# Kernel optimization log

Measured on AMD Instinct MI355X. Metric: run time of the kernel, lower is better.

The kernel has to match this reference:

```python
import jax, jax.numpy as jnp
import numpy as np

D_IN = 1024
D_OUT = 1024
NUM_HEADS = 16
D_HEAD = D_OUT // NUM_HEADS


def setup_inputs() -> dict:
    key = jax.random.key(0)
    ks = jax.random.split(key, 6)
    s = 0.02
    return {
        "x": jax.random.normal(ks[0], (2, 2048, D_IN), dtype=jnp.float32),
        "W_q": jax.random.normal(ks[1], (D_IN, D_OUT), dtype=jnp.float32) * s,
        "W_k": jax.random.normal(ks[2], (D_IN, D_OUT), dtype=jnp.float32) * s,
        "W_v": jax.random.normal(ks[3], (D_IN, D_OUT), dtype=jnp.float32) * s,
        "W_o": jax.random.normal(ks[4], (D_OUT, D_OUT), dtype=jnp.float32) * s,
        "b_o": jax.random.normal(ks[5], (D_OUT,), dtype=jnp.float32) * s,
    }


def reference(x, W_q, W_k, W_v, W_o, b_o):
    B, T, _ = x.shape
    # qkv projections (no bias), split heads -> [B, H, T, d_head]
    def split_heads(t):
        return t.reshape(B, T, NUM_HEADS, D_HEAD).transpose(0, 2, 1, 3)
    q = split_heads(x @ W_q)
    k = split_heads(x @ W_k)
    v = split_heads(x @ W_v)
    # full causal scores [B, H, T, T]
    scores = jnp.einsum("bhqd,bhkd->bhqk", q, k)
    causal = jnp.triu(jnp.ones((T, T), dtype=bool), k=1)
    scores = jnp.where(causal, -jnp.inf, scores)
    attn = jax.nn.softmax(scores / np.sqrt(D_HEAD).astype(np.float32), axis=-1)
    # dropout rate is 0.0 -> identity
    ctx = jnp.einsum("bhqk,bhkd->bhqd", attn, v)
    ctx = ctx.transpose(0, 2, 1, 3).reshape(B, T, D_OUT)
    return ctx @ W_o + b_o
```

## Files before the change

### kernel.cpp

```cpp
#include <hip/hip_runtime.h>
#include <hip/hip_bf16.h>
#include <cstdint>

#define SEQ_T 2048
#define DMODEL 1024
#define NHEAD 16
#define DHEAD 64

typedef __attribute__((ext_vector_type(8))) __bf16 bf16x8;
typedef __attribute__((ext_vector_type(4))) float floatx4;
typedef __attribute__((ext_vector_type(16))) float floatx16;
typedef __attribute__((ext_vector_type(2))) unsigned uint32x2;

static __device__ __forceinline__ uint16_t f2bf(float f) {
    union { float f; uint32_t u; } v; v.f = f;
    uint32_t r = v.u + 0x7FFFu + ((v.u >> 16) & 1u);
    return (uint16_t)(r >> 16);
}

static __device__ __forceinline__ uint32_t pack2bf(float a, float b) {
    union { __bf16 h[2]; uint32_t u; } p;
    p.h[0] = (__bf16)a; p.h[1] = (__bf16)b;
    return p.u;
}

__global__ void mha_cvt(const float* __restrict__ x, uint16_t* __restrict__ xb,
                        const float* __restrict__ W0, const float* __restrict__ W1,
                        const float* __restrict__ W2, const float* __restrict__ W3,
                        uint16_t* __restrict__ T0, uint16_t* __restrict__ T1,
                        uint16_t* __restrict__ T2, uint16_t* __restrict__ T3) {
    if (blockIdx.z == 4) {
        int base = (blockIdx.y * 16 + blockIdx.x) * 256 + threadIdx.x;
#pragma unroll
        for (int i = 0; i < 16; ++i) {
            int idx = base + i * 65536;
            float4 f = ((const float4*)x)[idx];
            union { uint16_t u[4]; uint64_t v; } o;
            o.u[0] = f2bf(f.x); o.u[1] = f2bf(f.y); o.u[2] = f2bf(f.z); o.u[3] = f2bf(f.w);
            ((uint64_t*)xb)[idx] = o.v;
        }
        return;
    }
    const float* W; uint16_t* Tt; float sc;
    switch (blockIdx.z) {
        case 0: W = W0; Tt = T0; sc = 0.125f * 1.44269504089f; break;
        case 1: W = W1; Tt = T1; sc = 1.f; break;
        case 2: W = W2; Tt = T2; sc = 1.f; break;
        default: W = W3; Tt = T3; sc = 1.f; break;
    }
    __shared__ float tile[64][65];
    const int c  = threadIdx.x & 63;
    const int r0 = threadIdx.x >> 6;
    const int R0 = blockIdx.y * 64, C0 = blockIdx.x * 64;
#pragma unroll
    for (int rr = 0; rr < 16; ++rr) {
        int r = r0 + rr * 4;
        tile[r][c] = W[(size_t)(R0 + r) * DMODEL + C0 + c];
    }
    __syncthreads();
#pragma unroll
    for (int rr = 0; rr < 16; ++rr) {
        int r = r0 + rr * 4;
        Tt[(size_t)(C0 + r) * DMODEL + R0 + c] = f2bf(tile[c][r] * sc);
    }
}

template<int MODE>
__device__ __forceinline__ void gemm_bk64_body(
    const uint16_t* __restrict__ A, const uint16_t* __restrict__ Bt,
    uint16_t* __restrict__ outB) {
    const int K = DMODEL, N = DMODEL;
    extern __shared__ char smem[];
    uint16_t* As = (uint16_t*)smem;
    uint16_t* Bs = (uint16_t*)(smem + 8192);
    const int tid  = threadIdx.x;
    const int wave = tid >> 6;
    const int lane = tid & 63;
    const int m0 = blockIdx.y * 64;
    const int n0 = blockIdx.x * 128;
    const int lr   = lane & 15;
    const int quad = lane >> 4;

    floatx4 acc[4][2];
#pragma unroll
    for (int i = 0; i < 4; ++i)
#pragma unroll
        for (int j = 0; j < 2; ++j) acc[i][j] = (floatx4)0.0f;

    for (int k0 = 0; k0 < K; k0 += 64) {
#pragma unroll
        for (int i = 0; i < 2; ++i) {
            int c = i * 256 + tid;
            int r = c >> 3, s = (c & 7) ^ (r & 7);
            const uint16_t* g = A + (size_t)(m0 + r) * K + k0 + s * 8;
            __builtin_amdgcn_global_load_lds((const __attribute__((address_space(1))) void*)g,
                                             (__attribute__((address_space(3))) void*)(As + (size_t)c * 8), 16, 0, 0);
        }
#pragma unroll
        for (int i = 0; i < 4; ++i) {
            int c = i * 256 + tid;
            int r = c >> 3, s = (c & 7) ^ (r & 7);
            const uint16_t* g = Bt + (size_t)(n0 + r) * K + k0 + s * 8;
            __builtin_amdgcn_global_load_lds((const __attribute__((address_space(1))) void*)g,
                                             (__attribute__((address_space(3))) void*)(Bs + (size_t)c * 8), 16, 0, 0);
        }
        __syncthreads();
#pragma unroll
        for (int ks = 0; ks < 2; ++ks) {
            bf16x8 af[4], bfr[2];
#pragma unroll
            for (int mi = 0; mi < 4; ++mi) {
                int row = mi * 16 + lr;
                af[mi] = *(const bf16x8*)&As[row * 64 + (((ks * 4 + quad) ^ (row & 7)) << 3)];
            }
#pragma unroll
            for (int ni = 0; ni < 2; ++ni) {
                int row = wave * 32 + ni * 16 + lr;
                bfr[ni] = *(const bf16x8*)&Bs[row * 64 + (((ks * 4 + quad) ^ (row & 7)) << 3)];
            }
#pragma unroll
            for (int mi = 0; mi < 4; ++mi)
#pragma unroll
                for (int ni = 0; ni < 2; ++ni)
                    acc[mi][ni] = __builtin_amdgcn_mfma_f32_16x16x32_bf16(af[mi], bfr[ni], acc[mi][ni], 0, 0, 0);
        }
        __syncthreads();
    }
    if constexpr (MODE == 1) {
        uint16_t* Ct = (uint16_t*)smem;
        const int bb = m0 >> 11, t0 = m0 & 2047;
#pragma unroll
        for (int mi = 0; mi < 4; ++mi)
#pragma unroll
            for (int ni = 0; ni < 2; ++ni) {
                int cl = wave * 32 + ni * 16 + lr;
                int tl = mi * 16 + quad * 4;
                int tls = tl ^ ((cl & 3) << 4);
                union { uint16_t u[4]; uint64_t v8; } pk;
#pragma unroll
                for (int r = 0; r < 4; ++r) pk.u[r] = f2bf(acc[mi][ni][r]);
                *(uint64_t*)&Ct[cl * 72 + tls] = pk.v8;
            }
        __syncthreads();
#pragma unroll
        for (int k = 0; k < 4; ++k) {
            int c = k * 256 + tid;
            int cl = c >> 3, off = (c & 7) * 8;
            int offs = off ^ ((cl & 3) << 4);
            uint4 v = *(const uint4*)&Ct[cl * 72 + offs];
            *(uint4*)&outB[((size_t)(bb * 1024 + n0 + cl)) * 2048 + t0 + off] = v;
        }
    } else {
#pragma unroll
        for (int mi = 0; mi < 4; ++mi)
#pragma unroll
            for (int ni = 0; ni < 2; ++ni) {
                int col = n0 + wave * 32 + ni * 16 + lr;
#pragma unroll
                for (int r = 0; r < 4; ++r) {
                    int row = m0 + mi * 16 + quad * 4 + r;
                    outB[(size_t)row * N + col] = f2bf(acc[mi][ni][r]);
                }
            }
    }
}

__global__ __launch_bounds__(256) void mha_gemm_qkv(
    const uint16_t* __restrict__ A,
    const uint16_t* __restrict__ Wq, const uint16_t* __restrict__ Wk, const uint16_t* __restrict__ Wv,
    uint16_t* __restrict__ Q, uint16_t* __restrict__ K, uint16_t* __restrict__ Vt) {
    switch (blockIdx.z) {
        case 0:  gemm_bk64_body<0>(A, Wq, Q);  break;
        case 1:  gemm_bk64_body<0>(A, Wk, K);  break;
        default: gemm_bk64_body<1>(A, Wv, Vt); break;
    }
}

__global__ __launch_bounds__(512) void mha_gemm_out(
    const uint16_t* __restrict__ A, const uint16_t* __restrict__ Wot,
    float* __restrict__ out, const float* __restrict__ bias) {
    const int K = DMODEL, N = DMODEL;
    extern __shared__ char smem[];
    uint16_t* As = (uint16_t*)smem;
    uint16_t* Bs = (uint16_t*)(smem + 8192);
    const int tid  = threadIdx.x;
    const int wave = tid >> 6;
    const int lane = tid & 63;
    const int m0 = blockIdx.y * 64;
    const int n0 = blockIdx.x * 128;
    const int lr   = lane & 15;
    const int quad = lane >> 4;
    const int wm = wave >> 2, wn = wave & 3;

    floatx4 acc[2][2];
#pragma unroll
    for (int i = 0; i < 2; ++i)
#pragma unroll
        for (int j = 0; j < 2; ++j) acc[i][j] = (floatx4)0.0f;

    for (int k0 = 0; k0 < K; k0 += 64) {
        {
            int c = tid;
            int r = c >> 3, s = (c & 7) ^ (r & 7);
            const uint16_t* g = A + (size_t)(m0 + r) * K + k0 + s * 8;
            __builtin_amdgcn_global_load_lds((const __attribute__((address_space(1))) void*)g,
                                             (__attribute__((address_space(3))) void*)(As + (size_t)c * 8), 16, 0, 0);
        }
#pragma unroll
        for (int i = 0; i < 2; ++i) {
            int c = i * 512 + tid;
            int r = c >> 3, s = (c & 7) ^ (r & 7);
            const uint16_t* g = Wot + (size_t)(n0 + r) * K + k0 + s * 8;
            __builtin_amdgcn_global_load_lds((const __attribute__((address_space(1))) void*)g,
                                             (__attribute__((address_space(3))) void*)(Bs + (size_t)c * 8), 16, 0, 0);
        }
        __syncthreads();
#pragma unroll
        for (int ks = 0; ks < 2; ++ks) {
            bf16x8 af[2], bfr[2];
#pragma unroll
            for (int mi = 0; mi < 2; ++mi) {
                int row = wm * 32 + mi * 16 + lr;
                af[mi] = *(const bf16x8*)&As[row * 64 + (((ks * 4 + quad) ^ (row & 7)) << 3)];
            }
#pragma unroll
            for (int ni = 0; ni < 2; ++ni) {
                int row = wn * 32 + ni * 16 + lr;
                bfr[ni] = *(const bf16x8*)&Bs[row * 64 + (((ks * 4 + quad) ^ (row & 7)) << 3)];
            }
#pragma unroll
            for (int mi = 0; mi < 2; ++mi)
#pragma unroll
                for (int ni = 0; ni < 2; ++ni)
                    acc[mi][ni] = __builtin_amdgcn_mfma_f32_16x16x32_bf16(af[mi], bfr[ni], acc[mi][ni], 0, 0, 0);
        }
        __syncthreads();
    }
#pragma unroll
    for (int mi = 0; mi < 2; ++mi)
#pragma unroll
        for (int ni = 0; ni < 2; ++ni) {
            int col = n0 + wn * 32 + ni * 16 + lr;
            float bv = bias[col];
#pragma unroll
            for (int r = 0; r < 4; ++r) {
                int row = m0 + wm * 32 + mi * 16 + quad * 4 + r;
                out[(size_t)row * N + col] = acc[mi][ni][r] + bv;
            }
        }
}

__global__ __launch_bounds__(256, 4) void mha_attn_mfma(
    const uint16_t* __restrict__ Q, const uint16_t* __restrict__ K,
    const uint16_t* __restrict__ Vt, uint16_t* __restrict__ ctx) {
    __shared__ alignas(16) uint16_t Ks[2][128 * 64];
    __shared__ alignas(16) uint16_t Vs[2][64 * 128];

    const int tid  = threadIdx.x;
    const int wave = tid >> 6;
    const int lane = tid & 63;
    const int l31  = lane & 31;
    const int hi   = lane >> 5;
    const int l7   = lane & 7;
    const int qg   = wave & 1;
    const int kvh  = wave >> 1;
    const int h = blockIdx.x;
    const int p = blockIdx.y;
    const int b = blockIdx.z;
    const int jH = 31 - p, jL = p;
    const int TH = (jH + 2) >> 1;

    const uint16_t* kg[4];
    const uint16_t* vg[4];
    int cch[4];
#pragma unroll
    for (int i = 0; i < 4; ++i) {
        int c = i * 256 + tid; cch[i] = c;
        int rk = c >> 3, ck = c & 7;
        kg[i] = K + ((size_t)(b * SEQ_T) + rk) * DMODEL + h * DHEAD + (ck ^ (rk & 7)) * 8;
        int rv = c >> 4, cv = c & 15;
        int sv = (cv & 8) | ((cv & 7) ^ (rv & 7));
        vg[i] = Vt + ((size_t)(b * 1024 + h * DHEAD + rv)) * 2048 + sv * 8;
    }

    int q0w = jH * 64 + qg * 32;
    bf16x8 qf[4];
    auto load_q = [&]() {
        const uint16_t* qb = Q + ((size_t)(b * SEQ_T) + q0w + l31) * DMODEL + h * DHEAD;
#pragma unroll
        for (int f = 0; f < 4; ++f)
            qf[f] = *(const bf16x8*)(qb + f * 16 + hi * 8);
    };
    load_q();

    floatx16 o[2];
#pragma unroll
    for (int dt = 0; dt < 2; ++dt) o[dt] = (floatx16)0.0f;
    float lac = 0.f;

    auto stage = [&](int kv0, int buf) {
#pragma unroll
        for (int i = 0; i < 4; ++i) {
            __builtin_amdgcn_global_load_lds(
                (const __attribute__((address_space(1))) void*)(kg[i] + (size_t)kv0 * DMODEL),
                (__attribute__((address_space(3))) void*)(&Ks[buf][cch[i] * 8]), 16, 0, 0);
            __builtin_amdgcn_global_load_lds(
                (const __attribute__((address_space(1))) void*)(vg[i] + kv0),
                (__attribute__((address_space(3))) void*)(&Vs[buf][cch[i] * 8]), 16, 0, 0);
        }
    };

    auto halfsum = [&](float x) -> float {
#if __has_builtin(__builtin_amdgcn_permlane32_swap)
        uint32x2 r = __builtin_amdgcn_permlane32_swap(__float_as_uint(x), __float_as_uint(x), false, false);
        return __uint_as_float(r.x) + __uint_as_float(r.y);
#else
        return x + __shfl_xor(x, 32, 64);
#endif
    };

    auto combine_store = [&](int cur) {
        __syncthreads();
        float* osc = (float*)&Vs[cur][0];
        float* lsc = (float*)&Ks[cur][0];
        float lt = halfsum(lac);
        if (kvh == 1) {
            if (lane < 32) lsc[qg * 32 + lane] = lt;
#pragma unroll
            for (int dt = 0; dt < 2; ++dt)
#pragma unroll
                for (int r = 0; r < 16; ++r) {
                    int row = (r & 3) + 8 * (r >> 2) + 4 * hi;
                    osc[(qg * 32 + row) * 64 + dt * 32 + l31] = o[dt][r];
                }
        }
        __syncthreads();
        if (kvh == 0) {
            float ltot = lt + lsc[qg * 32 + l31];
            if (lane < 32) lsc[64 + qg * 32 + lane] = 1.f / ltot;
#pragma unroll
            for (int dt = 0; dt < 2; ++dt)
#pragma unroll
                for (int r = 0; r < 16; ++r) {
                    int row = (r & 3) + 8 * (r >> 2) + 4 * hi;
                    float ov = o[dt][r] + osc[(qg * 32 + row) * 64 + dt * 32 + l31];
                    float li = lsc[64 + qg * 32 + row];
                    size_t addr = ((size_t)(b * SEQ_T) + q0w + row) * DMODEL + h * DHEAD + dt * 32 + l31;
                    ctx[addr] = f2bf(ov * li);
                }
        }
    };

    stage(0, 0);
    __syncthreads();

    for (int t = 0; t < 17; ++t) {
        const int cur = t & 1;
        const int kv0 = (t < TH ? t : t - TH) * 128;
        if (t + 1 < 17) {
            int tn = t + 1;
            stage((tn < TH ? tn : tn - TH) * 128, tn & 1);
        }
#pragma unroll
        for (int kt = 0; kt < 2; ++kt) {
            const int kb = kv0 + kvh * 64 + kt * 32;
            floatx16 s = (floatx16)0.0f;
#pragma unroll
            for (int f = 0; f < 4; ++f) {
                bf16x8 kf = *(const bf16x8*)&Ks[cur][(kvh * 64 + kt * 32 + l31) * 64 + (((2 * f + hi) ^ l7) << 3)];
                s = __builtin_amdgcn_mfma_f32_32x32x16_bf16(kf, qf[f], s, 0, 0, 0);
            }
            if (kb + 31 > q0w) {
                int qr = q0w + l31;
#pragma unroll
                for (int r = 0; r < 16; ++r) {
                    int k = kb + (r & 3) + 8 * (r >> 2) + 4 * hi;
                    if (k > qr) s[r] = -3e38f;
                }
            }
            float se[16];
#pragma unroll
            for (int r = 0; r < 16; ++r) {
                se[r] = __builtin_amdgcn_exp2f(s[r]);
                lac += se[r];
            }
            uint32_t d0[2], d1[2], d2[2], d3[2];
#pragma unroll
            for (int i = 0; i < 2; ++i) {
                d0[i] = pack2bf(se[2 * i],      se[2 * i + 1]);
                d1[i] = pack2bf(se[4 + 2 * i],  se[4 + 2 * i + 1]);
                d2[i] = pack2bf(se[8 + 2 * i],  se[8 + 2 * i + 1]);
                d3[i] = pack2bf(se[12 + 2 * i], se[12 + 2 * i + 1]);
            }
            bf16x8 paf[2];
#if __has_builtin(__builtin_amdgcn_permlane32_swap)
            {
                uint32x2 r0 = __builtin_amdgcn_permlane32_swap(d0[0], d1[0], false, false);
                uint32x2 r1 = __builtin_amdgcn_permlane32_swap(d0[1], d1[1], false, false);
                union { uint32_t u[4]; bf16x8 v; } f0;
                f0.u[0] = r0.x; f0.u[1] = r1.x; f0.u[2] = r0.y; f0.u[3] = r1.y;
                paf[0] = f0.v;
                uint32x2 r2 = __builtin_amdgcn_permlane32_swap(d2[0], d3[0], false, false);
                uint32x2 r3 = __builtin_amdgcn_permlane32_swap(d2[1], d3[1], false, false);
                union { uint32_t u[4]; bf16x8 v; } f1;
                f1.u[0] = r2.x; f1.u[1] = r3.x; f1.u[2] = r2.y; f1.u[3] = r3.y;
                paf[1] = f1.v;
            }
#else
            {
                uint32_t s00 = __shfl_xor((int)d0[0], 32, 64), s01 = __shfl_xor((int)d0[1], 32, 64);
                uint32_t s10 = __shfl_xor((int)d1[0], 32, 64), s11 = __shfl_xor((int)d1[1], 32, 64);
                union { uint32_t u[4]; bf16x8 v; } f0;
                f0.u[0] = hi ? s10 : d0[0]; f0.u[1] = hi ? s11 : d0[1];
                f0.u[2] = hi ? d1[0] : s00; f0.u[3] = hi ? d1[1] : s01;
                paf[0] = f0.v;
                uint32_t s20 = __shfl_xor((int)d2[0], 32, 64), s21 = __shfl_xor((int)d2[1], 32, 64);
                uint32_t s30 = __shfl_xor((int)d3[0], 32, 64), s31 = __shfl_xor((int)d3[1], 32, 64);
                union { uint32_t u[4]; bf16x8 v; } f1;
                f1.u[0] = hi ? s30 : d2[0]; f1.u[1] = hi ? s31 : d2[1];
                f1.u[2] = hi ? d3[0] : s20; f1.u[3] = hi ? d3[1] : s21;
                paf[1] = f1.v;
            }
#endif
#pragma unroll
            for (int f = 0; f < 2; ++f)
#pragma unroll
                for (int dt = 0; dt < 2; ++dt) {
                    bf16x8 vf = *(const bf16x8*)&Vs[cur][(dt * 32 + l31) * 128 + ((kvh * 8 + ((kt * 4 + 2 * f + hi) ^ l7)) << 3)];
                    o[dt] = __builtin_amdgcn_mfma_f32_32x32x16_bf16(paf[f], vf, o[dt], 0, 0, 0);
                }
        }
        if (t == TH - 1) {
            combine_store(cur);
            q0w = jL * 64 + qg * 32;
            load_q();
#pragma unroll
            for (int dt = 0; dt < 2; ++dt) o[dt] = (floatx16)0.0f;
            lac = 0.f;
        }
        if (t + 1 < 17) __syncthreads();
    }
    combine_store(0);
}

extern "C" void kernel_launch(void* const* d_in, const int* in_sizes, int n_in,
                              void* d_out, int out_size, void* d_ws, size_t ws_size,
                              hipStream_t stream) {
    const float* x  = (const float*)d_in[0];
    const float* Wq = (const float*)d_in[1];
    const float* Wk = (const float*)d_in[2];
    const float* Wv = (const float*)d_in[3];
    const float* Wo = (const float*)d_in[4];
    const float* bo = (const float*)d_in[5];
    float* out = (float*)d_out;

    char* ws = (char*)d_ws;
    const size_t SZ_X = (size_t)4096 * DMODEL * 2;
    const size_t SZ_W = (size_t)DMODEL * DMODEL * 2;
    size_t off = 0;
    uint16_t* xb  = (uint16_t*)(ws + off); off += SZ_X;
    uint16_t* wqt = (uint16_t*)(ws + off); off += SZ_W;
    uint16_t* wkt = (uint16_t*)(ws + off); off += SZ_W;
    uint16_t* wvt = (uint16_t*)(ws + off); off += SZ_W;
    uint16_t* wot = (uint16_t*)(ws + off); off += SZ_W;
    uint16_t* Qb  = (uint16_t*)(ws + off); off += SZ_X;
    uint16_t* Kb  = (uint16_t*)(ws + off); off += SZ_X;
    uint16_t* Vtb = (uint16_t*)(ws + off); off += SZ_X;
    uint16_t* Cb  = (uint16_t*)(ws + off); off += SZ_X;
    (void)ws_size; (void)in_sizes; (void)n_in; (void)out_size;

    mha_cvt<<<dim3(16, 16, 5), 256, 0, stream>>>(x, xb, Wq, Wk, Wv, Wo, wqt, wkt, wvt, wot);
    mha_gemm_qkv<<<dim3(8, 64, 3), 256, 24576, stream>>>(xb, wqt, wkt, wvt, Qb, Kb, Vtb);
    mha_attn_mfma<<<dim3(NHEAD, 16, 2), 256, 0, stream>>>(Qb, Kb, Vtb, Cb);
    mha_gemm_out<<<dim3(8, 64), 512, 24576, stream>>>(Cb, wot, out, bo);
}
```

Before: 175.1 us.

## Split attention KV tile across four wave pairs with 512-thread blocks

The attention kernel now runs 8 waves per block instead of 4. Each 128-key tile is split into four 32-key slices, one per wave pair, and each wave now handles a single 32-key sub-tile per iteration instead of two. Partial outputs and row sums are reduced through LDS in three serialized passes. It also wraps the MFMA sections in s_setprio to favour matrix issue. The aim is more waves in flight to hide latency, at the cost of a longer cross-wave reduction, more barriers and possibly lower occupancy from 64KB of dynamic LDS per block.

```diff
diff --git a/kernel.cpp b/kernel.cpp
--- a/kernel.cpp
+++ b/kernel.cpp
@@ -250,11 +250,12 @@
         }
 }
 
-__global__ __launch_bounds__(256, 4) void mha_attn_mfma(
+__global__ __launch_bounds__(512, 4) void mha_attn_mfma(
     const uint16_t* __restrict__ Q, const uint16_t* __restrict__ K,
     const uint16_t* __restrict__ Vt, uint16_t* __restrict__ ctx) {
-    __shared__ alignas(16) uint16_t Ks[2][128 * 64];
-    __shared__ alignas(16) uint16_t Vs[2][64 * 128];
+    extern __shared__ char asmem[];
+    uint16_t* Ks0 = (uint16_t*)asmem;
+    uint16_t* Vs0 = (uint16_t*)(asmem + 32768);
 
     const int tid  = threadIdx.x;
     const int wave = tid >> 6;
@@ -263,21 +264,21 @@
     const int hi   = lane >> 5;
     const int l7   = lane & 7;
     const int qg   = wave & 1;
-    const int kvh  = wave >> 1;
+    const int kvq  = wave >> 1;
     const int h = blockIdx.x;
     const int p = blockIdx.y;
     const int b = blockIdx.z;
     const int jH = 31 - p, jL = p;
-    const int TH = (jH + 2) >> 1;
-
-    const uint16_t* kg[4];
-    const uint16_t* vg[4];
-    int cch[4];
-#pragma unroll
-    for (int i = 0; i < 4; ++i) {
-        int c = i * 256 + tid; cch[i] = c;
+    const int TH = (33 - p) >> 1;
+
+    const uint16_t* kg[2];
+    const uint16_t* vg[2];
+    int cch[2];
+#pragma unroll
+    for (int i = 0; i < 2; ++i) {
+        int c = i * 512 + tid; cch[i] = c;
         int rk = c >> 3, ck = c & 7;
-        kg[i] = K + ((size_t)(b * SEQ_T) + rk) * DMODEL + h * DHEAD + (ck ^ (rk & 7)) * 8;
+        kg[i] = K + ((size_t)(b * SEQ_T) + rk) * DMODEL + h * DHEAD + ((ck ^ (rk & 7)) * 8);
         int rv = c >> 4, cv = c & 15;
         int sv = (cv & 8) | ((cv & 7) ^ (rv & 7));
         vg[i] = Vt + ((size_t)(b * 1024 + h * DHEAD + rv)) * 2048 + sv * 8;
@@ -299,14 +300,16 @@
     float lac = 0.f;
 
     auto stage = [&](int kv0, int buf) {
-#pragma unroll
-        for (int i = 0; i < 4; ++i) {
+        uint16_t* kd = Ks0 + buf * 8192;
+        uint16_t* vd = Vs0 + buf * 8192;
+#pragma unroll
+        for (int i = 0; i < 2; ++i) {
             __builtin_amdgcn_global_load_lds(
                 (const __attribute__((address_space(1))) void*)(kg[i] + (size_t)kv0 * DMODEL),
-                (__attribute__((address_space(3))) void*)(&Ks[buf][cch[i] * 8]), 16, 0, 0);
+                (__attribute__((address_space(3))) void*)(kd + cch[i] * 8), 16, 0, 0);
             __builtin_amdgcn_global_load_lds(
                 (const __attribute__((address_space(1))) void*)(vg[i] + kv0),
-                (__attribute__((address_space(3))) void*)(&Vs[buf][cch[i] * 8]), 16, 0, 0);
+                (__attribute__((address_space(3))) void*)(vd + cch[i] * 8), 16, 0, 0);
         }
     };
 
@@ -321,21 +324,35 @@
 
     auto combine_store = [&](int cur) {
         __syncthreads();
-        float* osc = (float*)&Vs[cur][0];
-        float* lsc = (float*)&Ks[cur][0];
+        float* osc = (float*)(Ks0 + cur * 8192);
+        float* lsc = (float*)(Vs0 + cur * 8192);
         float lt = halfsum(lac);
-        if (kvh == 1) {
-            if (lane < 32) lsc[qg * 32 + lane] = lt;
-#pragma unroll
-            for (int dt = 0; dt < 2; ++dt)
-#pragma unroll
-                for (int r = 0; r < 16; ++r) {
-                    int row = (r & 3) + 8 * (r >> 2) + 4 * hi;
-                    osc[(qg * 32 + row) * 64 + dt * 32 + l31] = o[dt][r];
+#pragma unroll
+        for (int pass = 3; pass >= 1; --pass) {
+            if (kvq == pass) {
+                if (pass == 3) {
+#pragma unroll
+                    for (int dt = 0; dt < 2; ++dt)
+#pragma unroll
+                        for (int r = 0; r < 16; ++r) {
+                            int row = (r & 3) + 8 * (r >> 2) + 4 * hi;
+                            osc[(qg * 32 + row) * 64 + dt * 32 + l31] = o[dt][r];
+                        }
+                    if (lane < 32) lsc[qg * 32 + lane] = lt;
+                } else {
+#pragma unroll
+                    for (int dt = 0; dt < 2; ++dt)
+#pragma unroll
+                        for (int r = 0; r < 16; ++r) {
+                            int row = (r & 3) + 8 * (r >> 2) + 4 * hi;
+                            osc[(qg * 32 + row) * 64 + dt * 32 + l31] += o[dt][r];
+                        }
+                    if (lane < 32) lsc[qg * 32 + lane] += lt;
                 }
-        }
-        __syncthreads();
-        if (kvh == 0) {
+            }
+            __syncthreads();
+        }
+        if (kvq == 0) {
             float ltot = lt + lsc[qg * 32 + l31];
             if (lane < 32) lsc[64 + qg * 32 + lane] = 1.f / ltot;
 #pragma unroll
@@ -361,75 +378,78 @@
             int tn = t + 1;
             stage((tn < TH ? tn : tn - TH) * 128, tn & 1);
         }
-#pragma unroll
-        for (int kt = 0; kt < 2; ++kt) {
-            const int kb = kv0 + kvh * 64 + kt * 32;
-            floatx16 s = (floatx16)0.0f;
-#pragma unroll
-            for (int f = 0; f < 4; ++f) {
-                bf16x8 kf = *(const bf16x8*)&Ks[cur][(kvh * 64 + kt * 32 + l31) * 64 + (((2 * f + hi) ^ l7) << 3)];
-                s = __builtin_amdgcn_mfma_f32_32x32x16_bf16(kf, qf[f], s, 0, 0, 0);
-            }
-            if (kb + 31 > q0w) {
-                int qr = q0w + l31;
-#pragma unroll
-                for (int r = 0; r < 16; ++r) {
-                    int k = kb + (r & 3) + 8 * (r >> 2) + 4 * hi;
-                    if (k > qr) s[r] = -3e38f;
-                }
-            }
-            float se[16];
+        const uint16_t* Kc = Ks0 + cur * 8192;
+        const uint16_t* Vc = Vs0 + cur * 8192;
+        const int kb = kv0 + kvq * 32;
+        floatx16 s = (floatx16)0.0f;
+        __builtin_amdgcn_s_setprio(1);
+#pragma unroll
+        for (int f = 0; f < 4; ++f) {
+            bf16x8 kf = *(const bf16x8*)&Kc[(kvq * 32 + l31) * 64 + (((2 * f + hi) ^ l7) << 3)];
+            s = __builtin_amdgcn_mfma_f32_32x32x16_bf16(kf, qf[f], s, 0, 0, 0);
+        }
+        __builtin_amdgcn_s_setprio(0);
+        if (kb + 31 > q0w) {
+            int qr = q0w + l31;
 #pragma unroll
             for (int r = 0; r < 16; ++r) {
-                se[r] = __builtin_amdgcn_exp2f(s[r]);
-                lac += se[r];
-            }
-            uint32_t d0[2], d1[2], d2[2], d3[2];
-#pragma unroll
-            for (int i = 0; i < 2; ++i) {
-                d0[i] = pack2bf(se[2 * i],      se[2 * i + 1]);
-                d1[i] = pack2bf(se[4 + 2 * i],  se[4 + 2 * i + 1]);
-                d2[i] = pack2bf(se[8 + 2 * i],  se[8 + 2 * i + 1]);
-                d3[i] = pack2bf(se[12 + 2 * i], se[12 + 2 * i + 1]);
-            }
-            bf16x8 paf[2];
+                int k = kb + (r & 3) + 8 * (r >> 2) + 4 * hi;
+                if (k > qr) s[r] = -3e38f;
+            }
+        }
+        float se[16];
+#pragma unroll
+        for (int r = 0; r < 16; ++r) {
+            se[r] = __builtin_amdgcn_exp2f(s[r]);
+            lac += se[r];
+        }
+        uint32_t d0[2], d1[2], d2[2], d3[2];
+#pragma unroll
+        for (int i = 0; i < 2; ++i) {
+            d0[i] = pack2bf(se[2 * i],      se[2 * i + 1]);
+            d1[i] = pack2bf(se[4 + 2 * i],  se[4 + 2 * i + 1]);
+            d2[i] = pack2bf(se[8 + 2 * i],  se[8 + 2 * i + 1]);
+            d3[i] = pack2bf(se[12 + 2 * i], se[12 + 2 * i + 1]);
+        }
+        bf16x8 paf[2];
 #if __has_builtin(__builtin_amdgcn_permlane32_swap)
-            {
-                uint32x2 r0 = __builtin_amdgcn_permlane32_swap(d0[0], d1[0], false, false);
-                uint32x2 r1 = __builtin_amdgcn_permlane32_swap(d0[1], d1[1], false, false);
-                union { uint32_t u[4]; bf16x8 v; } f0;
-                f0.u[0] = r0.x; f0.u[1] = r1.x; f0.u[2] = r0.y; f0.u[3] = r1.y;
-                paf[0] = f0.v;
-                uint32x2 r2 = __builtin_amdgcn_permlane32_swap(d2[0], d3[0], false, false);
-                uint32x2 r3 = __builtin_amdgcn_permlane32_swap(d2[1], d3[1], false, false);
-                union { uint32_t u[4]; bf16x8 v; } f1;
-                f1.u[0] = r2.x; f1.u[1] = r3.x; f1.u[2] = r2.y; f1.u[3] = r3.y;
-                paf[1] = f1.v;
-            }
+        {
+            uint32x2 r0 = __builtin_amdgcn_permlane32_swap(d0[0], d1[0], false, false);
+            uint32x2 r1 = __builtin_amdgcn_permlane32_swap(d0[1], d1[1], false, false);
+            union { uint32_t u[4]; bf16x8 v; } f0;
+            f0.u[0] = r0.x; f0.u[1] = r1.x; f0.u[2] = r0.y; f0.u[3] = r1.y;
+            paf[0] = f0.v;
+            uint32x2 r2 = __builtin_amdgcn_permlane32_swap(d2[0], d3[0], false, false);
+            uint32x2 r3 = __builtin_amdgcn_permlane32_swap(d2[1], d3[1], false, false);
+            union { uint32_t u[4]; bf16x8 v; } f1;
+            f1.u[0] = r2.x; f1.u[1] = r3.x; f1.u[2] = r2.y; f1.u[3] = r3.y;
+            paf[1] = f1.v;
+        }
 #else
-            {
-                uint32_t s00 = __shfl_xor((int)d0[0], 32, 64), s01 = __shfl_xor((int)d0[1], 32, 64);
-                uint32_t s10 = __shfl_xor((int)d1[0], 32, 64), s11 = __shfl_xor((int)d1[1], 32, 64);
-                union { uint32_t u[4]; bf16x8 v; } f0;
-                f0.u[0] = hi ? s10 : d0[0]; f0.u[1] = hi ? s11 : d0[1];
-                f0.u[2] = hi ? d1[0] : s00; f0.u[3] = hi ? d1[1] : s01;
-                paf[0] = f0.v;
-                uint32_t s20 = __shfl_xor((int)d2[0], 32, 64), s21 = __shfl_xor((int)d2[1], 32, 64);
-                uint32_t s30 = __shfl_xor((int)d3[0], 32, 64), s31 = __shfl_xor((int)d3[1], 32, 64);
-                union { uint32_t u[4]; bf16x8 v; } f1;
-                f1.u[0] = hi ? s30 : d2[0]; f1.u[1] = hi ? s31 : d2[1];
-                f1.u[2] = hi ? d3[0] : s20; f1.u[3] = hi ? d3[1] : s21;
-                paf[1] = f1.v;
-            }
+        {
+            uint32_t s00 = __shfl_xor((int)d0[0], 32, 64), s01 = __shfl_xor((int)d0[1], 32, 64);
+            uint32_t s10 = __shfl_xor((int)d1[0], 32, 64), s11 = __shfl_xor((int)d1[1], 32, 64);
+            union { uint32_t u[4]; bf16x8 v; } f0;
+            f0.u[0] = hi ? s10 : d0[0]; f0.u[1] = hi ? s11 : d0[1];
+            f0.u[2] = hi ? d1[0] : s00; f0.u[3] = hi ? d1[1] : s01;
+            paf[0] = f0.v;
+            uint32_t s20 = __shfl_xor((int)d2[0], 32, 64), s21 = __shfl_xor((int)d2[1], 32, 64);
+            uint32_t s30 = __shfl_xor((int)d3[0], 32, 64), s31 = __shfl_xor((int)d3[1], 32, 64);
+            union { uint32_t u[4]; bf16x8 v; } f1;
+            f1.u[0] = hi ? s30 : d2[0]; f1.u[1] = hi ? s31 : d2[1];
+            f1.u[2] = hi ? d3[0] : s20; f1.u[3] = hi ? d3[1] : s21;
+            paf[1] = f1.v;
+        }
 #endif
-#pragma unroll
-            for (int f = 0; f < 2; ++f)
-#pragma unroll
-                for (int dt = 0; dt < 2; ++dt) {
-                    bf16x8 vf = *(const bf16x8*)&Vs[cur][(dt * 32 + l31) * 128 + ((kvh * 8 + ((kt * 4 + 2 * f + hi) ^ l7)) << 3)];
-                    o[dt] = __builtin_amdgcn_mfma_f32_32x32x16_bf16(paf[f], vf, o[dt], 0, 0, 0);
-                }
-        }
+        __builtin_amdgcn_s_setprio(1);
+#pragma unroll
+        for (int f = 0; f < 2; ++f)
+#pragma unroll
+            for (int dt = 0; dt < 2; ++dt) {
+                bf16x8 vf = *(const bf16x8*)&Vc[(dt * 32 + l31) * 128 + (((kvq * 4 + 2 * f + hi) ^ l7) << 3)];
+                o[dt] = __builtin_amdgcn_mfma_f32_32x32x16_bf16(paf[f], vf, o[dt], 0, 0, 0);
+            }
+        __builtin_amdgcn_s_setprio(0);
         if (t == TH - 1) {
             combine_store(cur);
             q0w = jL * 64 + qg * 32;
@@ -471,6 +491,6 @@
 
     mha_cvt<<<dim3(16, 16, 5), 256, 0, stream>>>(x, xb, Wq, Wk, Wv, Wo, wqt, wkt, wvt, wot);
     mha_gemm_qkv<<<dim3(8, 64, 3), 256, 24576, stream>>>(xb, wqt, wkt, wvt, Qb, Kb, Vtb);
-    mha_attn_mfma<<<dim3(NHEAD, 16, 2), 256, 0, stream>>>(Qb, Kb, Vtb, Cb);
+    mha_attn_mfma<<<dim3(NHEAD, 16, 2), 512, 65536, stream>>>(Qb, Kb, Vtb, Cb);
     mha_gemm_out<<<dim3(8, 64), 512, 24576, stream>>>(Cb, wot, out, bo);
 }
```

Measured after the change: 181.4 us. +3.6%, slower.
